# Performance work log

Hardware: AMD Instinct MI355X
Metric: run time of the kernel (lower is better)

Reference implementation:

```python
import jax, jax.numpy as jnp
import numpy as np

MAX_NEIGHBORS = 10
D = 1024
N = 16384

def setup_inputs() -> dict:
    key = jax.random.key(0)
    ks = jax.random.split(key, 12)
    s = 0.05
    inp = {
        'target_embedding': jax.random.normal(ks[0], (D,), jnp.float32),
        'all_embeddings': jax.random.normal(ks[1], (N, D), jnp.float32),
        'similarity_matrix': jax.random.normal(ks[2], (N, N), jnp.float32),
        # attention_net: Linear(2D->D), ReLU, Linear(D->1)
        'W_att1': jax.random.normal(ks[3], (2 * D, D), jnp.float32) * s,
        'b_att1': jnp.zeros((D,), jnp.float32),
        'W_att2': jax.random.normal(ks[4], (D, 1), jnp.float32) * s,
        'b_att2': jnp.zeros((1,), jnp.float32),
        # neighbor_count_net: Linear(D->D//2), ReLU, Linear(D//2->1), Sigmoid
        'W_cnt1': jax.random.normal(ks[5], (D, D // 2), jnp.float32) * s,
        'b_cnt1': jnp.zeros((D // 2,), jnp.float32),
        'W_cnt2': jax.random.normal(ks[6], (D // 2, 1), jnp.float32) * s,
        'b_cnt2': jnp.zeros((1,), jnp.float32),
        'target_idx': 123,
    }
    return inp

def reference(target_embedding, all_embeddings, similarity_matrix,
              W_att1, b_att1, W_att2, b_att2,
              W_cnt1, b_cnt1, W_cnt2, b_cnt2, target_idx):
    # dynamic neighbor count: int(sigmoid(mlp(x)) * max_neighbors), clamped to [1, max_neighbors]
    h = jax.nn.relu(target_embedding @ W_cnt1 + b_cnt1)
    frac = jax.nn.sigmoid(h @ W_cnt2 + b_cnt2)[0]
    dynamic_k = jnp.clip(jnp.floor(frac * MAX_NEIGHBORS).astype(jnp.int32), 1, MAX_NEIGHBORS)

    # top-(K+1) over the target's similarity row; statically sized, mask to dynamic_k
    row = similarity_matrix[target_idx]
    _, top_idx = jax.lax.top_k(row, MAX_NEIGHBORS + 1)  # [K+1]
    # stable compaction: move target_idx (if present) to the end, keep order otherwise
    order = jnp.where(top_idx == target_idx, MAX_NEIGHBORS + 1, jnp.arange(MAX_NEIGHBORS + 1))
    neighbor_idx = top_idx[jnp.argsort(order)][:MAX_NEIGHBORS]  # [K]
    valid = jnp.arange(MAX_NEIGHBORS) < dynamic_k              # [K]

    neighbor_emb = all_embeddings[neighbor_idx]                 # [K, D]
    target_exp = jnp.broadcast_to(target_embedding, (MAX_NEIGHBORS, D))
    pair = jnp.concatenate([target_exp, neighbor_emb], axis=-1)  # [K, 2D]
    scores = (jax.nn.relu(pair @ W_att1 + b_att1) @ W_att2 + b_att2)[:, 0]  # [K]
    scores = jnp.where(valid, scores, -jnp.inf)
    weights = jax.nn.softmax(scores)                            # zeros at invalid slots
    aggregated = weights @ neighbor_emb                         # [D]
    return aggregated, weights, neighbor_idx, weights
```

## Files before the change

kernel.cpp:

```cpp
#include <hip/hip_runtime.h>
#include <math.h>

#define NN 16384
#define DD 1024
#define HD 512

#define WS_DK  0
#define WS_NB  4
#define WS_SC  16
#define WS_UP  64
#define WS_HP  (64 + 32 * 1024)

__global__ void __launch_bounds__(256) k1(const float* __restrict__ x,
                                          const float* __restrict__ W1,
                                          const float* __restrict__ Wc1,
                                          const float* __restrict__ sim,
                                          const int* __restrict__ tidx,
                                          float* __restrict__ ws,
                                          float* __restrict__ out) {
    const int t = threadIdx.x;
    const int b = blockIdx.x;
    const int lane = t & 63, wave = t >> 6;

    if (b > 0 && b <= 64) {
        __shared__ float xs[32];
        const int idx = b - 1, ic = idx >> 1, jc = idx & 1;
        const int ibase = ic * 32;
        if (t < 32) xs[t] = x[ibase + t];
        __syncthreads();
        #pragma unroll
        for (int jj = 0; jj < 2; ++jj) {
            const int j = jc * 512 + jj * 256 + t;
            float acc = 0.f;
            const float* W = W1 + (size_t)ibase * DD + j;
            #pragma unroll 8
            for (int ii = 0; ii < 32; ++ii) acc += xs[ii] * W[(size_t)ii * DD];
            ws[WS_UP + ic * DD + j] = acc;
        }
        return;
    }
    if (b > 64) {
        __shared__ float xs[32];
        const int c = b - 65;
        const int ibase = c * 32;
        if (t < 32) xs[t] = x[ibase + t];
        __syncthreads();
        #pragma unroll
        for (int jj = 0; jj < 2; ++jj) {
            const int j = t + jj * 256;
            float acc = 0.f;
            const float* W = Wc1 + (size_t)ibase * HD + j;
            #pragma unroll 8
            for (int ii = 0; ii < 32; ++ii) acc += xs[ii] * W[(size_t)ii * HD];
            ws[WS_HP + c * HD + j] = acc;
        }
        return;
    }

    if (t < 10) ws[WS_SC + t] = 0.f;

    const int tgt = tidx[0];
    const float4* row4 = (const float4*)(sim + (size_t)tgt * NN);
    float vals[64];
    #pragma unroll
    for (int c = 0; c < 16; ++c) {
        float4 v = row4[c * 256 + t];
        vals[c * 4 + 0] = v.x; vals[c * 4 + 1] = v.y;
        vals[c * 4 + 2] = v.z; vals[c * 4 + 3] = v.w;
    }
    float bv = -INFINITY; int bs = 0;
    #pragma unroll
    for (int s = 0; s < 64; ++s) if (vals[s] > bv) { bv = vals[s]; bs = s; }

    __shared__ float wvs[4];
    __shared__ int   wgs[4];
    __shared__ int   winner;
    __shared__ int   toplist[11];

    for (int it = 0; it < 11; ++it) {
        float cv = bv;
        int   cg = (bs >> 2) * 1024 + t * 4 + (bs & 3);
        for (int off = 32; off > 0; off >>= 1) {
            float ov = __shfl_down(cv, off);
            int   og = __shfl_down(cg, off);
            if (ov > cv || (ov == cv && og < cg)) { cv = ov; cg = og; }
        }
        if (lane == 0) { wvs[wave] = cv; wgs[wave] = cg; }
        __syncthreads();
        if (t == 0) {
            float fv = wvs[0]; int fg = wgs[0];
            for (int w = 1; w < 4; ++w)
                if (wvs[w] > fv || (wvs[w] == fv && wgs[w] < fg)) { fv = wvs[w]; fg = wgs[w]; }
            toplist[it] = fg;
            winner = fg;
        }
        __syncthreads();
        const int w = winner;
        if (((w >> 2) & 255) == t) {
            vals[((w >> 10) << 2) | (w & 3)] = -INFINITY;
            bv = -INFINITY; bs = 0;
            #pragma unroll
            for (int s = 0; s < 64; ++s) if (vals[s] > bv) { bv = vals[s]; bs = s; }
        }
    }
    if (t == 0) {
        int cnt = 0;
        int* nbp = (int*)ws + WS_NB;
        for (int i = 0; i < 11 && cnt < 10; ++i) {
            int v = toplist[i];
            if (v != tgt) { nbp[cnt] = v; out[1034 + cnt] = (float)v; ++cnt; }
        }
    }
}

__global__ void __launch_bounds__(512) k2(const float* __restrict__ emb,
                                          const float* __restrict__ W1,
                                          const float* __restrict__ ba1,
                                          const float* __restrict__ W2,
                                          const float* __restrict__ bc1,
                                          const float* __restrict__ Wc2,
                                          const float* __restrict__ bc2,
                                          float* __restrict__ ws) {
    const int t = threadIdx.x;
    const int b = blockIdx.x;

    __shared__ int    nb[10];
    __shared__ float4 es4[10][256];
    __shared__ float  red[16][32][11];
    __shared__ float  ucol[32];
    __shared__ float  scr[32][10];
    __shared__ float  redc[512];

    if (b == 32) {
        const int j = t;
        float s = 0.f;
        #pragma unroll 8
        for (int c = 0; c < 32; ++c) s += ws[WS_HP + c * HD + j];
        float h = fmaxf(s + bc1[j], 0.f);
        redc[t] = h * Wc2[j];
        __syncthreads();
        for (int off = 256; off > 0; off >>= 1) {
            if (t < off) redc[t] += redc[t + off];
            __syncthreads();
        }
        if (t == 0) {
            float z = redc[0] + bc2[0];
            float frac = 1.f / (1.f + expf(-z));
            int dk = (int)floorf(frac * 10.f);
            ((int*)ws)[WS_DK] = dk < 1 ? 1 : (dk > 10 ? 10 : dk);
        }
        return;
    }

    const int jl  = t & 31;
    const int seg = t >> 5;
    const int jg  = b * 32 + jl;

    if (t < 10) nb[t] = ((const int*)ws)[WS_NB + t];
    __syncthreads();
    for (int i = t; i < 2560; i += 512) {
        int k = i >> 8, c = i & 255;
        es4[k][c] = ((const float4*)(emb + (size_t)nb[k] * DD))[c];
    }
    if (t < 32) {
        float s = 0.f;
        #pragma unroll 8
        for (int ic = 0; ic < 32; ++ic) s += ws[WS_UP + ic * DD + b * 32 + t];
        ucol[t] = s;
    }
    __syncthreads();

    float acc[10];
    #pragma unroll
    for (int k = 0; k < 10; ++k) acc[k] = 0.f;
    const float* Wb = W1 + (size_t)(1024 + seg * 64) * DD + jg;
    for (int c = 0; c < 16; ++c) {
        float4 ev[10];
        #pragma unroll
        for (int k = 0; k < 10; ++k) ev[k] = es4[k][seg * 16 + c];
        #pragma unroll
        for (int q = 0; q < 4; ++q) {
            const float wb = Wb[(size_t)(c * 4 + q) * DD];
            #pragma unroll
            for (int k = 0; k < 10; ++k)
                acc[k] += reinterpret_cast<const float*>(&ev[k])[q] * wb;
        }
    }
    #pragma unroll
    for (int k = 0; k < 10; ++k) red[seg][jl][k] = acc[k];
    __syncthreads();

    if (t < 32) {
        const float u  = ucol[t];
        const float bj = ba1[b * 32 + t];
        const float w2 = W2[b * 32 + t];
        #pragma unroll
        for (int k = 0; k < 10; ++k) {
            float s = 0.f;
            #pragma unroll
            for (int g = 0; g < 16; ++g) s += red[g][t][k];
            scr[t][k] = fmaxf(u + s + bj, 0.f) * w2;
        }
    }
    __syncthreads();
    if (t < 10) {
        float s = 0.f;
        #pragma unroll 8
        for (int c = 0; c < 32; ++c) s += scr[c][t];
        atomicAdd(&ws[WS_SC + t], s);
    }
}

__global__ void __launch_bounds__(1024) k3(const float* __restrict__ emb,
                                           const float* __restrict__ ba2,
                                           float* __restrict__ ws,
                                           float* __restrict__ out) {
    const int t = threadIdx.x;
    __shared__ float wl[10];
    __shared__ int   nb[10];
    if (t < 10) nb[t] = ((const int*)ws)[WS_NB + t];
    if (t == 0) {
        const int dk = ((const int*)ws)[WS_DK];
        float sv[10];
        float m = -INFINITY;
        for (int k = 0; k < 10; ++k) {
            float s = ws[WS_SC + k] + ba2[0];
            sv[k] = (k < dk) ? s : -INFINITY;
            if (sv[k] > m) m = sv[k];
        }
        float sum = 0.f;
        for (int k = 0; k < 10; ++k) { sv[k] = expf(sv[k] - m); sum += sv[k]; }
        for (int k = 0; k < 10; ++k) wl[k] = sv[k] / sum;
    }
    __syncthreads();
    float a = 0.f;
    #pragma unroll
    for (int k = 0; k < 10; ++k) a += wl[k] * emb[(size_t)nb[k] * DD + t];
    out[t] = a;
    if (t < 10) { out[1024 + t] = wl[t]; out[1044 + t] = wl[t]; }
}

extern "C" void kernel_launch(void* const* d_in, const int* in_sizes, int n_in,
                              void* d_out, int out_size, void* d_ws, size_t ws_size,
                              hipStream_t stream) {
    const float* x    = (const float*)d_in[0];
    const float* emb  = (const float*)d_in[1];
    const float* sim  = (const float*)d_in[2];
    const float* W1   = (const float*)d_in[3];
    const float* ba1  = (const float*)d_in[4];
    const float* W2   = (const float*)d_in[5];
    const float* ba2  = (const float*)d_in[6];
    const float* Wc1  = (const float*)d_in[7];
    const float* bc1  = (const float*)d_in[8];
    const float* Wc2  = (const float*)d_in[9];
    const float* bc2  = (const float*)d_in[10];
    const int*   tidx = (const int*)d_in[11];
    float* out = (float*)d_out;
    float* ws  = (float*)d_ws;

    hipLaunchKernelGGL(k1, dim3(97), dim3(256),  0, stream, x, W1, Wc1, sim, tidx, ws, out);
    hipLaunchKernelGGL(k2, dim3(33), dim3(512),  0, stream, emb, W1, ba1, W2, bc1, Wc2, bc2, ws);
    hipLaunchKernelGGL(k3, dim3(1),  dim3(1024), 0, stream, emb, ba2, ws, out);
}
```

Baseline: 41.22 us.

## Replace block-synchronized top-k with per-wave lists merged once; widen k2 grid

The top-k block now uses 512 threads. Each wave independently extracts its own top-11 candidates with shuffles only, and thread 0 merges the eight per-wave lists at the end, which removes the two block barriers per iteration. k2 doubles its grid to 64 column blocks of 16 columns each, spreading the W1 second-half reads over more CUs. The column-sum reduction is parallelized across 160 threads, and the count-net reduction uses wave shuffles. The cost is more redundant per-wave work and a serial 8-way merge on one thread.

Result: faster. 38.42 us (median of 2 runs) (-6.8%).

```diff
diff --git a/kernel.cpp b/kernel.cpp
--- a/kernel.cpp
+++ b/kernel.cpp
@@ -11,7 +11,7 @@
 #define WS_UP  64
 #define WS_HP  (64 + 32 * 1024)
 
-__global__ void __launch_bounds__(256) k1(const float* __restrict__ x,
+__global__ void __launch_bounds__(512) k1(const float* __restrict__ x,
                                           const float* __restrict__ W1,
                                           const float* __restrict__ Wc1,
                                           const float* __restrict__ sim,
@@ -28,15 +28,12 @@
         const int ibase = ic * 32;
         if (t < 32) xs[t] = x[ibase + t];
         __syncthreads();
-        #pragma unroll
-        for (int jj = 0; jj < 2; ++jj) {
-            const int j = jc * 512 + jj * 256 + t;
-            float acc = 0.f;
-            const float* W = W1 + (size_t)ibase * DD + j;
-            #pragma unroll 8
-            for (int ii = 0; ii < 32; ++ii) acc += xs[ii] * W[(size_t)ii * DD];
-            ws[WS_UP + ic * DD + j] = acc;
-        }
+        const int j = jc * 512 + t;
+        float acc = 0.f;
+        const float* W = W1 + (size_t)ibase * DD + j;
+        #pragma unroll 8
+        for (int ii = 0; ii < 32; ++ii) acc += xs[ii] * W[(size_t)ii * DD];
+        ws[WS_UP + ic * DD + j] = acc;
         return;
     }
     if (b > 64) {
@@ -45,15 +42,11 @@
         const int ibase = c * 32;
         if (t < 32) xs[t] = x[ibase + t];
         __syncthreads();
-        #pragma unroll
-        for (int jj = 0; jj < 2; ++jj) {
-            const int j = t + jj * 256;
-            float acc = 0.f;
-            const float* W = Wc1 + (size_t)ibase * HD + j;
-            #pragma unroll 8
-            for (int ii = 0; ii < 32; ++ii) acc += xs[ii] * W[(size_t)ii * HD];
-            ws[WS_HP + c * HD + j] = acc;
-        }
+        float acc = 0.f;
+        const float* W = Wc1 + (size_t)ibase * HD + t;
+        #pragma unroll 8
+        for (int ii = 0; ii < 32; ++ii) acc += xs[ii] * W[(size_t)ii * HD];
+        ws[WS_HP + c * HD + t] = acc;
         return;
     }
 
@@ -61,49 +54,57 @@
 
     const int tgt = tidx[0];
     const float4* row4 = (const float4*)(sim + (size_t)tgt * NN);
-    float vals[64];
-    #pragma unroll
-    for (int c = 0; c < 16; ++c) {
-        float4 v = row4[c * 256 + t];
+    float vals[32];
+    #pragma unroll
+    for (int c = 0; c < 8; ++c) {
+        float4 v = row4[c * 512 + t];
         vals[c * 4 + 0] = v.x; vals[c * 4 + 1] = v.y;
         vals[c * 4 + 2] = v.z; vals[c * 4 + 3] = v.w;
     }
+    unsigned used = 0u;
     float bv = -INFINITY; int bs = 0;
     #pragma unroll
-    for (int s = 0; s < 64; ++s) if (vals[s] > bv) { bv = vals[s]; bs = s; }
-
-    __shared__ float wvs[4];
-    __shared__ int   wgs[4];
-    __shared__ int   winner;
-    __shared__ int   toplist[11];
+    for (int s = 0; s < 32; ++s) if (vals[s] > bv) { bv = vals[s]; bs = s; }
+
+    __shared__ float wlv[8][11];
+    __shared__ int   wli[8][11];
 
     for (int it = 0; it < 11; ++it) {
         float cv = bv;
-        int   cg = (bs >> 2) * 1024 + t * 4 + (bs & 3);
+        int   cg = (bs >> 2) * 2048 + t * 4 + (bs & 3);
+        #pragma unroll
         for (int off = 32; off > 0; off >>= 1) {
             float ov = __shfl_down(cv, off);
             int   og = __shfl_down(cg, off);
             if (ov > cv || (ov == cv && og < cg)) { cv = ov; cg = og; }
         }
-        if (lane == 0) { wvs[wave] = cv; wgs[wave] = cg; }
-        __syncthreads();
-        if (t == 0) {
-            float fv = wvs[0]; int fg = wgs[0];
-            for (int w = 1; w < 4; ++w)
-                if (wvs[w] > fv || (wvs[w] == fv && wgs[w] < fg)) { fv = wvs[w]; fg = wgs[w]; }
+        const int wg = __shfl(cg, 0);
+        if (lane == 0) { wlv[wave][it] = cv; wli[wave][it] = cg; }
+        if (((wg >> 2) & 511) == t) {
+            used |= 1u << (((wg >> 11) << 2) | (wg & 3));
+            bv = -INFINITY; bs = 0;
+            #pragma unroll
+            for (int s = 0; s < 32; ++s) {
+                float v = ((used >> s) & 1u) ? -INFINITY : vals[s];
+                if (v > bv) { bv = v; bs = s; }
+            }
+        }
+    }
+    __syncthreads();
+    if (t == 0) {
+        int head[8] = {0, 0, 0, 0, 0, 0, 0, 0};
+        int toplist[11];
+        for (int it = 0; it < 11; ++it) {
+            float fv = -INFINITY; int fg = 0x7fffffff; int fw = 0;
+            #pragma unroll
+            for (int w = 0; w < 8; ++w) {
+                float v = wlv[w][head[w]];
+                int   g = wli[w][head[w]];
+                if (v > fv || (v == fv && g < fg)) { fv = v; fg = g; fw = w; }
+            }
             toplist[it] = fg;
-            winner = fg;
-        }
-        __syncthreads();
-        const int w = winner;
-        if (((w >> 2) & 255) == t) {
-            vals[((w >> 10) << 2) | (w & 3)] = -INFINITY;
-            bv = -INFINITY; bs = 0;
-            #pragma unroll
-            for (int s = 0; s < 64; ++s) if (vals[s] > bv) { bv = vals[s]; bs = s; }
-        }
-    }
-    if (t == 0) {
+            head[fw] = head[fw] < 10 ? head[fw] + 1 : 10;
+        }
         int cnt = 0;
         int* nbp = (int*)ws + WS_NB;
         for (int i = 0; i < 11 && cnt < 10; ++i) {
@@ -123,28 +124,28 @@
                                           float* __restrict__ ws) {
     const int t = threadIdx.x;
     const int b = blockIdx.x;
+    const int lane = t & 63, wave = t >> 6;
 
     __shared__ int    nb[10];
     __shared__ float4 es4[10][256];
-    __shared__ float  red[16][32][11];
-    __shared__ float  ucol[32];
-    __shared__ float  scr[32][10];
-    __shared__ float  redc[512];
-
-    if (b == 32) {
-        const int j = t;
+    __shared__ float  red[32][16][11];
+    __shared__ float  ured[32][17];
+    __shared__ float  scr[16][10];
+    __shared__ float  redp[8];
+
+    if (b == 64) {
         float s = 0.f;
         #pragma unroll 8
-        for (int c = 0; c < 32; ++c) s += ws[WS_HP + c * HD + j];
-        float h = fmaxf(s + bc1[j], 0.f);
-        redc[t] = h * Wc2[j];
+        for (int c = 0; c < 32; ++c) s += ws[WS_HP + c * HD + t];
+        float v = fmaxf(s + bc1[t], 0.f) * Wc2[t];
+        #pragma unroll
+        for (int off = 32; off > 0; off >>= 1) v += __shfl_down(v, off);
+        if (lane == 0) redp[wave] = v;
         __syncthreads();
-        for (int off = 256; off > 0; off >>= 1) {
-            if (t < off) redc[t] += redc[t + off];
-            __syncthreads();
-        }
         if (t == 0) {
-            float z = redc[0] + bc2[0];
+            float z = bc2[0];
+            #pragma unroll
+            for (int w = 0; w < 8; ++w) z += redp[w];
             float frac = 1.f / (1.f + expf(-z));
             int dk = (int)floorf(frac * 10.f);
             ((int*)ws)[WS_DK] = dk < 1 ? 1 : (dk > 10 ? 10 : dk);
@@ -152,32 +153,28 @@
         return;
     }
 
-    const int jl  = t & 31;
-    const int seg = t >> 5;
-    const int jg  = b * 32 + jl;
+    const int jl  = t & 15;
+    const int seg = t >> 4;
+    const int jg  = b * 16 + jl;
 
     if (t < 10) nb[t] = ((const int*)ws)[WS_NB + t];
     __syncthreads();
+    #pragma unroll
     for (int i = t; i < 2560; i += 512) {
         int k = i >> 8, c = i & 255;
         es4[k][c] = ((const float4*)(emb + (size_t)nb[k] * DD))[c];
     }
-    if (t < 32) {
-        float s = 0.f;
-        #pragma unroll 8
-        for (int ic = 0; ic < 32; ++ic) s += ws[WS_UP + ic * DD + b * 32 + t];
-        ucol[t] = s;
-    }
+    ured[seg][jl] = ws[WS_UP + seg * DD + jg];
     __syncthreads();
 
     float acc[10];
     #pragma unroll
     for (int k = 0; k < 10; ++k) acc[k] = 0.f;
-    const float* Wb = W1 + (size_t)(1024 + seg * 64) * DD + jg;
-    for (int c = 0; c < 16; ++c) {
+    const float* Wb = W1 + (size_t)(1024 + seg * 32) * DD + jg;
+    for (int c = 0; c < 8; ++c) {
         float4 ev[10];
         #pragma unroll
-        for (int k = 0; k < 10; ++k) ev[k] = es4[k][seg * 16 + c];
+        for (int k = 0; k < 10; ++k) ev[k] = es4[k][seg * 8 + c];
         #pragma unroll
         for (int q = 0; q < 4; ++q) {
             const float wb = Wb[(size_t)(c * 4 + q) * DD];
@@ -190,23 +187,21 @@
     for (int k = 0; k < 10; ++k) red[seg][jl][k] = acc[k];
     __syncthreads();
 
-    if (t < 32) {
-        const float u  = ucol[t];
-        const float bj = ba1[b * 32 + t];
-        const float w2 = W2[b * 32 + t];
-        #pragma unroll
-        for (int k = 0; k < 10; ++k) {
-            float s = 0.f;
-            #pragma unroll
-            for (int g = 0; g < 16; ++g) s += red[g][t][k];
-            scr[t][k] = fmaxf(u + s + bj, 0.f) * w2;
-        }
+    if (t < 160) {
+        const int k = t >> 4, jj = t & 15;
+        float s = 0.f;
+        #pragma unroll 8
+        for (int g = 0; g < 32; ++g) s += red[g][jj][k];
+        float u = 0.f;
+        #pragma unroll 8
+        for (int g = 0; g < 32; ++g) u += ured[g][jj];
+        scr[jj][k] = fmaxf(u + s + ba1[b * 16 + jj], 0.f) * W2[b * 16 + jj];
     }
     __syncthreads();
     if (t < 10) {
         float s = 0.f;
-        #pragma unroll 8
-        for (int c = 0; c < 32; ++c) s += scr[c][t];
+        #pragma unroll
+        for (int c = 0; c < 16; ++c) s += scr[c][t];
         atomicAdd(&ws[WS_SC + t], s);
     }
 }
@@ -258,7 +253,7 @@
     float* out = (float*)d_out;
     float* ws  = (float*)d_ws;
 
-    hipLaunchKernelGGL(k1, dim3(97), dim3(256),  0, stream, x, W1, Wc1, sim, tidx, ws, out);
-    hipLaunchKernelGGL(k2, dim3(33), dim3(512),  0, stream, emb, W1, ba1, W2, bc1, Wc2, bc2, ws);
+    hipLaunchKernelGGL(k1, dim3(97), dim3(512),  0, stream, x, W1, Wc1, sim, tidx, ws, out);
+    hipLaunchKernelGGL(k2, dim3(65), dim3(512),  0, stream, emb, W1, ba1, W2, bc1, Wc2, bc2, ws);
     hipLaunchKernelGGL(k3, dim3(1),  dim3(1024), 0, stream, emb, ba2, ws, out);
 }
```
